# Kernel optimization log

Measured on AMD Instinct MI355X. Metric: run time of the kernel, lower is better.

Reference implementation:

```python
import jax, jax.numpy as jnp
import numpy as np

B, C, H, W = 8, 64, 64, 64
OUT_H, OUT_W = 32, 32


def setup_inputs() -> dict:
    key = jax.random.key(0)
    ks = jax.random.split(key, 9)
    s = 1.0 / np.sqrt(C).astype(np.float32)
    return {
        "x": jax.random.normal(ks[0], (B, C, H, W), jnp.float32),
        "wq": jax.random.normal(ks[1], (C, C), jnp.float32) * s,
        "bq": jax.random.normal(ks[2], (C,), jnp.float32) * 0.01,
        "wk": jax.random.normal(ks[3], (C, C), jnp.float32) * s,
        "bk": jax.random.normal(ks[4], (C,), jnp.float32) * 0.01,
        "wv": jax.random.normal(ks[5], (C, C), jnp.float32) * s,
        "bv": jax.random.normal(ks[6], (C,), jnp.float32) * 0.01,
        "wm": jax.random.normal(ks[7], (C, C), jnp.float32) * s,
        "bm": jax.random.normal(ks[8], (C,), jnp.float32) * 0.01,
    }


def reference(x, wq, bq, wk, bk, wv, bv, wm, bm):
    # pushforward: self-attention over spatial tokens, 1x1-conv mixing + ReLU,
    # then bilinear resize to out_shape (align_corners=False semantics).
    b, c, h, w = x.shape
    t = x.reshape(b, c, h * w).transpose(0, 2, 1)  # [B, HW, C] tokens
    q = jnp.einsum('bnc,dc->bnd', t, wq) + bq      # 1x1 conv == per-pixel linear
    k = jnp.einsum('bnc,dc->bnd', t, wk) + bk
    v = jnp.einsum('bnc,dc->bnd', t, wv) + bv
    scores = jnp.einsum('bnc,bmc->bnm', q, k) / jnp.sqrt(jnp.float32(c))  # [B, HW, HW]
    attn = jax.nn.softmax(scores, axis=-1)
    o = jnp.einsum('bnm,bmc->bnc', attn, v)        # [B, HW, C]
    mixed = jax.nn.relu(jnp.einsum('bnc,dc->bnd', o, wm) + bm)
    out = mixed.transpose(0, 2, 1).reshape(b, c, h, w)
    # F.interpolate(mode='bilinear', align_corners=False) == half-pixel bilinear, no antialias
    out = jax.image.resize(out, (b, c, OUT_H, OUT_W), method='bilinear', antialias=False)
    return out
```

## Files before the change

### kernel.cpp

```cpp
#include <hip/hip_runtime.h>
#include <stdint.h>

typedef unsigned short u16;
typedef unsigned int   u32;
typedef __attribute__((ext_vector_type(8)))  short short8;
typedef __attribute__((ext_vector_type(4)))  float f32x4;
typedef __attribute__((ext_vector_type(16))) float f32x16;

#define NTOK 4096
#define LOG2E 1.44269504088896340736f
#define QS    (0.125f * LOG2E)

__device__ __forceinline__ u16 f2bf(float f) {
    u32 u = __builtin_bit_cast(u32, f);
    u += 0x7fffu + ((u >> 16) & 1u);
    return (u16)(u >> 16);
}
__device__ __forceinline__ float bf2f(u16 v) {
    return __builtin_bit_cast(float, (u32)v << 16);
}
__device__ __forceinline__ u32 pk_hu(float a, float b) {
    u32 ua = __builtin_bit_cast(u32, a) + 0x8000u;
    u32 ub = __builtin_bit_cast(u32, b) + 0x8000u;
    return __builtin_amdgcn_perm(ub, ua, 0x07060302);
}
__device__ __forceinline__ f32x16 zero16() {
    f32x16 v;
#pragma unroll
    for (int i = 0; i < 16; ++i) v[i] = 0.f;
    return v;
}

#define MFMA16x32 __builtin_amdgcn_mfma_f32_16x16x32_bf16
#define MFMA32x16 __builtin_amdgcn_mfma_f32_32x32x16_bf16

__global__ __launch_bounds__(256) void qkv_mfma4(
    const float* __restrict__ x,
    const float* __restrict__ wq, const float* __restrict__ bq,
    const float* __restrict__ wk, const float* __restrict__ bk,
    const float* __restrict__ wv, const float* __restrict__ bv,
    u16* __restrict__ Q, u16* __restrict__ K, u16* __restrict__ Vp)
{
    __shared__ __align__(16) u16 Wl[3 * 64 * 72];
    __shared__ __align__(16) u16 Xl[64 * 64];
    const int tid  = threadIdx.x;
    const int b    = blockIdx.x & 7;
    const int slab = blockIdx.x >> 3;
    const int n0   = slab << 6;
    const int wave = tid >> 6;
    const int lane = tid & 63;
    const int quad = lane >> 4;
    const int l15  = lane & 15;

#pragma unroll
    for (int j = 0; j < 12; ++j) {
        const float* src = (j < 4) ? wq : (j < 8) ? wk : wv;
        const float sc = (j < 4) ? QS : 1.0f;
        const int idx = (j & 3) * 1024 + tid * 4;
        const float4 v = *(const float4*)(src + idx);
        uint2 pk;
        pk.x = (u32)f2bf(v.x * sc) | ((u32)f2bf(v.y * sc) << 16);
        pk.y = (u32)f2bf(v.z * sc) | ((u32)f2bf(v.w * sc) << 16);
        *(uint2*)&Wl[(j >> 2) * 4608 + (idx >> 6) * 72 + (idx & 63)] = pk;
    }

    float4 xs[4];
#pragma unroll
    for (int g = 0; g < 4; ++g) {
        const int ch = g * 16 + wave * 4 + quad;
        xs[g] = *(const float4*)(x + ((size_t)(b * 64 + ch)) * NTOK + n0 + l15 * 4);
    }
#pragma unroll
    for (int g = 0; g < 4; ++g) {
        const int ch = g * 16 + wave * 4 + quad;
        const float vv[4] = {xs[g].x, xs[g].y, xs[g].z, xs[g].w};
#pragma unroll
        for (int e = 0; e < 4; ++e) {
            const int tok = l15 * 4 + e;
            Xl[tok * 64 + (((ch >> 3) ^ (tok & 7)) & 7) * 8 + (ch & 7)] = f2bf(vv[e]);
        }
    }
    __syncthreads();

    const int row0 = wave * 16 + l15;
    short8 xf[2];
#pragma unroll
    for (int kk = 0; kk < 2; ++kk)
        xf[kk] = *(const short8*)&Xl[row0 * 64 + (((kk * 4 + quad) ^ (row0 & 7)) & 7) * 8];

    const size_t tokbase = (size_t)b * NTOK + n0 + wave * 16;

#pragma unroll
    for (int mat = 0; mat < 2; ++mat) {
        const float* bias = (mat == 0) ? bq : bk;
        const float bsc = (mat == 0) ? QS : 1.0f;
#pragma unroll
        for (int mt = 0; mt < 4; ++mt) {
            const u16* wr = &Wl[mat * 4608 + (mt * 16 + l15) * 72 + quad * 8];
            const short8 wf0 = *(const short8*)(wr);
            const short8 wf1 = *(const short8*)(wr + 32);
            f32x4 acc = {0.f, 0.f, 0.f, 0.f};
            acc = MFMA16x32(wf0, xf[0], acc, 0, 0, 0);
            acc = MFMA16x32(wf1, xf[1], acc, 0, 0, 0);
            const float4 b4 = *(const float4*)(bias + mt * 16 + quad * 4);
            uint2 pk;
            pk.x = (u32)f2bf(acc[0] + b4.x * bsc) | ((u32)f2bf(acc[1] + b4.y * bsc) << 16);
            pk.y = (u32)f2bf(acc[2] + b4.z * bsc) | ((u32)f2bf(acc[3] + b4.w * bsc) << 16);
            u16* dst = (mat == 0) ? Q : K;
            *(uint2*)(dst + (tokbase + l15) * 64 + mt * 16 + quad * 4) = pk;
        }
    }

    __syncthreads();
    u16* Vl = Xl;
    const int tok = wave * 16 + l15;
#pragma unroll
    for (int mt = 0; mt < 4; ++mt) {
        const u16* wr = &Wl[2 * 4608 + (mt * 16 + l15) * 72 + quad * 8];
        const short8 wf0 = *(const short8*)(wr);
        const short8 wf1 = *(const short8*)(wr + 32);
        f32x4 acc = {0.f, 0.f, 0.f, 0.f};
        acc = MFMA16x32(wf0, xf[0], acc, 0, 0, 0);
        acc = MFMA16x32(wf1, xf[1], acc, 0, 0, 0);
        const float4 b4 = *(const float4*)(bv + mt * 16 + quad * 4);
        const float o[4] = {acc[0] + b4.x, acc[1] + b4.y, acc[2] + b4.z, acc[3] + b4.w};
#pragma unroll
        for (int r = 0; r < 4; ++r) {
            const int d = mt * 16 + quad * 4 + r;
            Vl[d * 64 + (((tok >> 3) ^ ((d >> 1) & 7)) & 7) * 8 + (tok & 7)] = f2bf(o[r]);
        }
    }
    __syncthreads();

#pragma unroll
    for (int dd = 0; dd < 4; ++dd) {
        const int d2   = (tid >> 4) + dd * 16;
        const int tok0 = (tid & 15) * 4;
        const int slot = ((tok0 >> 3) ^ ((d2 >> 1) & 7)) & 7;
        const uint2 v2 = *(const uint2*)&Vl[d2 * 64 + slot * 8 + (tok0 & 7)];
        const int gt  = slab * 2 + (tok0 >> 5);
        const int tl  = tok0 & 31;
        const int sl  = (tl & 0x13) | (((tl >> 2) & 1) << 3) | (((tl >> 3) & 1) << 2);
        *(uint2*)(Vp + (((size_t)b * 128 + gt) * 64 + d2) * 32 + sl) = v2;
    }
}

__global__ __launch_bounds__(512, 2) void attn8(
    const u16* __restrict__ Q, const u16* __restrict__ K,
    const u16* __restrict__ Vp,
    const float* __restrict__ wm, const float* __restrict__ bm,
    float* __restrict__ out)
{
    __shared__ __align__(16) char smem[54272];
    const int tid  = threadIdx.x;
    const int wave = tid >> 6;
    const int lane = tid & 63;
    const int c31  = lane & 31;
    const int hw   = lane >> 5;
    const int quad = lane >> 4;
    const int l15  = lane & 15;
    const int h    = wave >> 2;
    const int s    = wave & 3;
    const int b    = blockIdx.x & 7;
    const int oh   = blockIdx.x >> 3;
    const int n0   = oh * 128;

    short8 qf[2][4];
#pragma unroll
    for (int nt = 0; nt < 2; ++nt)
#pragma unroll
        for (int ks = 0; ks < 4; ++ks)
            qf[nt][ks] = *(const short8*)(Q + ((size_t)(b * NTOK + n0 + h * 64 + nt * 32 + c31)) * 64
                                            + ks * 16 + hw * 8);

    const u16* Kb  = K + ((size_t)b * NTOK + s * 1024) * 64;
    const u16* Vbp = Vp + ((size_t)b * 128 + s * 32) * 2048;

    f32x16 O[2][2];
#pragma unroll
    for (int mt = 0; mt < 2; ++mt)
#pragma unroll
        for (int nt = 0; nt < 2; ++nt) O[mt][nt] = zero16();
    float lpa[2] = {0.f, 0.f};

    auto load_kv = [&](short8 (&kf)[4], short8 (&vf)[4], int t) {
        const int tc = (t < 32) ? t : 31;
        const u16* kt = Kb + (size_t)tc * 2048;
#pragma unroll
        for (int ks = 0; ks < 4; ++ks)
            kf[ks] = *(const short8*)(kt + c31 * 64 + ks * 16 + hw * 8);
        const u16* vt = Vbp + (size_t)tc * 2048;
#pragma unroll
        for (int mk = 0; mk < 4; ++mk)
            vf[mk] = *(const short8*)(vt + ((mk >> 1) * 32 + c31) * 32 + (mk & 1) * 16 + hw * 8);
    };

    auto S_compute = [&](f32x16 (&sv)[2], const short8 (&kf)[4]) {
#pragma unroll
        for (int nt = 0; nt < 2; ++nt) {
            f32x16 a = zero16();
            a = MFMA32x16(kf[0], qf[nt][0], a, 0, 0, 0);
            a = MFMA32x16(kf[1], qf[nt][1], a, 0, 0, 0);
            a = MFMA32x16(kf[2], qf[nt][2], a, 0, 0, 0);
            a = MFMA32x16(kf[3], qf[nt][3], a, 0, 0, 0);
            sv[nt] = a;
        }
    };

    auto tile_tail = [&](const f32x16 (&sv)[2], const short8 (&vf)[4]) {
#pragma unroll
        for (int nt = 0; nt < 2; ++nt) {
            float p[16];
#pragma unroll
            for (int r = 0; r < 16; ++r) p[r] = __builtin_amdgcn_exp2f(sv[nt][r]);
            lpa[nt] += (((p[0] + p[1]) + (p[2] + p[3])) + ((p[4] + p[5]) + (p[6] + p[7])))
                     + (((p[8] + p[9]) + (p[10] + p[11])) + ((p[12] + p[13]) + (p[14] + p[15])));
            uint4 B0, B1;
            B0.x = pk_hu(p[0],  p[1]);  B0.y = pk_hu(p[2],  p[3]);
            B0.z = pk_hu(p[4],  p[5]);  B0.w = pk_hu(p[6],  p[7]);
            B1.x = pk_hu(p[8],  p[9]);  B1.y = pk_hu(p[10], p[11]);
            B1.z = pk_hu(p[12], p[13]); B1.w = pk_hu(p[14], p[15]);
            const short8 pb0 = __builtin_bit_cast(short8, B0);
            const short8 pb1 = __builtin_bit_cast(short8, B1);
            O[0][nt] = MFMA32x16(vf[0], pb0, O[0][nt], 0, 0, 0);
            O[0][nt] = MFMA32x16(vf[1], pb1, O[0][nt], 0, 0, 0);
            O[1][nt] = MFMA32x16(vf[2], pb0, O[1][nt], 0, 0, 0);
            O[1][nt] = MFMA32x16(vf[3], pb1, O[1][nt], 0, 0, 0);
        }
    };

    short8 kfA[4], vfA[4], kfB[4], vfB[4];
    f32x16 svA[2], svB[2];
    load_kv(kfA, vfA, 0);
    load_kv(kfB, vfB, 1);
    S_compute(svA, kfA);

#pragma unroll 1
    for (int tt = 0; tt < 16; ++tt) {
        const int t0 = tt * 2;
        S_compute(svB, kfB);
        tile_tail(svA, vfA);
        load_kv(kfA, vfA, t0 + 2);
        S_compute(svA, kfA);
        tile_tail(svB, vfB);
        load_kv(kfB, vfB, t0 + 3);
    }

#pragma unroll
    for (int nt = 0; nt < 2; ++nt) lpa[nt] += __shfl_xor(lpa[nt], 32);

    float* lpbuf = (float*)(smem + 52224);
    if (hw == 0) {
#pragma unroll
        for (int nt = 0; nt < 2; ++nt)
            lpbuf[(h * 4 + s) * 64 + nt * 32 + c31] = lpa[nt];
    }
    if (s != 0) {
        u16* sec = (u16*)smem + (h * 3 + s - 1) * 4352;
#pragma unroll
        for (int mt = 0; mt < 2; ++mt)
#pragma unroll
            for (int nt = 0; nt < 2; ++nt)
#pragma unroll
                for (int r = 0; r < 16; ++r) {
                    const int ch = mt * 32 + (r & 3) + 8 * (r >> 2) + 4 * hw;
                    sec[(nt * 32 + c31) * 68 + ch] = f2bf(O[mt][nt][r]);
                }
    }
    __syncthreads();

    float rinv[2];
    if (s == 0) {
#pragma unroll
        for (int nt = 0; nt < 2; ++nt) {
            float sum = 0.f;
#pragma unroll
            for (int sx = 0; sx < 4; ++sx)
                sum += lpbuf[(h * 4 + sx) * 64 + nt * 32 + c31];
            rinv[nt] = 1.0f / sum;
        }
#pragma unroll
        for (int sx = 1; sx < 4; ++sx) {
            const u16* sec = (const u16*)smem + (h * 3 + sx - 1) * 4352;
#pragma unroll
            for (int mt = 0; mt < 2; ++mt)
#pragma unroll
                for (int nt = 0; nt < 2; ++nt)
#pragma unroll
                    for (int r = 0; r < 16; ++r) {
                        const int ch = mt * 32 + (r & 3) + 8 * (r >> 2) + 4 * hw;
                        O[mt][nt][r] += bf2f(sec[(nt * 32 + c31) * 68 + ch]);
                    }
        }
    }
    short8 wB[4][2];
    float bb[4];
#pragma unroll
    for (int nt = 0; nt < 4; ++nt) {
        const int d = nt * 16 + l15;
        const float* wr = wm + (size_t)d * 64 + quad * 8;
        const float4 a0 = *(const float4*)(wr);
        const float4 a1 = *(const float4*)(wr + 4);
        const float4 c0 = *(const float4*)(wr + 32);
        const float4 c1 = *(const float4*)(wr + 36);
        ((u32*)&wB[nt][0])[0] = (u32)f2bf(a0.x) | ((u32)f2bf(a0.y) << 16);
        ((u32*)&wB[nt][0])[1] = (u32)f2bf(a0.z) | ((u32)f2bf(a0.w) << 16);
        ((u32*)&wB[nt][0])[2] = (u32)f2bf(a1.x) | ((u32)f2bf(a1.y) << 16);
        ((u32*)&wB[nt][0])[3] = (u32)f2bf(a1.z) | ((u32)f2bf(a1.w) << 16);
        ((u32*)&wB[nt][1])[0] = (u32)f2bf(c0.x) | ((u32)f2bf(c0.y) << 16);
        ((u32*)&wB[nt][1])[1] = (u32)f2bf(c0.z) | ((u32)f2bf(c0.w) << 16);
        ((u32*)&wB[nt][1])[2] = (u32)f2bf(c1.x) | ((u32)f2bf(c1.y) << 16);
        ((u32*)&wB[nt][1])[3] = (u32)f2bf(c1.z) | ((u32)f2bf(c1.w) << 16);
        bb[nt] = bm[d];
    }
    __syncthreads();

    if (s == 0) {
        u16* M0 = (u16*)smem + h * 4096;
#pragma unroll
        for (int mt = 0; mt < 2; ++mt)
#pragma unroll
            for (int nt = 0; nt < 2; ++nt)
#pragma unroll
                for (int r = 0; r < 16; ++r) {
                    const int lr = nt * 32 + c31;
                    const int ch = mt * 32 + (r & 3) + 8 * (r >> 2) + 4 * hw;
                    const float v = O[mt][nt][r] * rinv[nt];
                    M0[lr * 64 + (((ch >> 3) ^ (lr & 7)) & 7) * 8 + (ch & 7)] = f2bf(v);
                }
    }
    __syncthreads();

    const u16* M0r = (const u16*)smem + (wave >> 2) * 4096;
    const int lr = (wave & 3) * 16 + l15;
    const short8 af0 = *(const short8*)&M0r[lr * 64 + ((quad ^ (lr & 7)) & 7) * 8];
    const short8 af1 = *(const short8*)&M0r[lr * 64 + (((4 + quad) ^ (lr & 7)) & 7) * 8];
    float* Mf = (float*)(smem + 16384);
#pragma unroll
    for (int nt = 0; nt < 4; ++nt) {
        f32x4 acc = {0.f, 0.f, 0.f, 0.f};
        acc = MFMA16x32(af0, wB[nt][0], acc, 0, 0, 0);
        acc = MFMA16x32(af1, wB[nt][1], acc, 0, 0, 0);
#pragma unroll
        for (int r = 0; r < 4; ++r) {
            float v = acc[r] + bb[nt];
            v = v > 0.f ? v : 0.f;
            Mf[(wave * 16 + quad * 4 + r) * 68 + nt * 16 + l15] = v;
        }
    }
    __syncthreads();

    const int ow = tid & 31;
    const int cb = (tid >> 5) & 15;
#pragma unroll
    for (int i = 0; i < 4; ++i) {
        const int c = cb + i * 16;
        const float v = 0.25f * (Mf[(2 * ow) * 68 + c] + Mf[(2 * ow + 1) * 68 + c]
                               + Mf[(64 + 2 * ow) * 68 + c] + Mf[(65 + 2 * ow) * 68 + c]);
        out[((size_t)(b * 64 + c) * 32 + oh) * 32 + ow] = v;
    }
}

extern "C" void kernel_launch(void* const* d_in, const int* in_sizes, int n_in,
                              void* d_out, int out_size, void* d_ws, size_t ws_size,
                              hipStream_t stream) {
    (void)in_sizes; (void)n_in; (void)out_size; (void)ws_size;
    const float* x  = (const float*)d_in[0];
    const float* wq = (const float*)d_in[1];
    const float* bq = (const float*)d_in[2];
    const float* wk = (const float*)d_in[3];
    const float* bk = (const float*)d_in[4];
    const float* wv = (const float*)d_in[5];
    const float* bv = (const float*)d_in[6];
    const float* wm = (const float*)d_in[7];
    const float* bm = (const float*)d_in[8];

    u16* Q  = (u16*)d_ws;
    u16* K  = Q + (size_t)8 * NTOK * 64;
    u16* Vp = K + (size_t)8 * NTOK * 64;

    qkv_mfma4<<<512, 256, 0, stream>>>(x, wq, bq, wk, bk, wv, bv, Q, K, Vp);
    attn8<<<256, 512, 0, stream>>>(Q, K, Vp, wm, bm, (float*)d_out);
}
```

Before: 136.2 us.

## Split attention block into 16 waves each owning 32 query rows

```diff
diff --git a/kernel.cpp b/kernel.cpp
--- a/kernel.cpp
+++ b/kernel.cpp
@@ -145,7 +145,7 @@
     }
 }
 
-__global__ __launch_bounds__(512, 2) void attn8(
+__global__ __launch_bounds__(1024, 4) void attn9(
     const u16* __restrict__ Q, const u16* __restrict__ K,
     const u16* __restrict__ Vp,
     const float* __restrict__ wm, const float* __restrict__ bm,
@@ -165,196 +165,171 @@
     const int oh   = blockIdx.x >> 3;
     const int n0   = oh * 128;
 
-    short8 qf[2][4];
-#pragma unroll
-    for (int nt = 0; nt < 2; ++nt)
-#pragma unroll
-        for (int ks = 0; ks < 4; ++ks)
-            qf[nt][ks] = *(const short8*)(Q + ((size_t)(b * NTOK + n0 + h * 64 + nt * 32 + c31)) * 64
-                                            + ks * 16 + hw * 8);
+    short8 qf[4];
+#pragma unroll
+    for (int ks = 0; ks < 4; ++ks)
+        qf[ks] = *(const short8*)(Q + ((size_t)(b * NTOK + n0 + h * 32 + c31)) * 64
+                                    + ks * 16 + hw * 8);
 
     const u16* Kb  = K + ((size_t)b * NTOK + s * 1024) * 64;
     const u16* Vbp = Vp + ((size_t)b * 128 + s * 32) * 2048;
 
-    f32x16 O[2][2];
-#pragma unroll
-    for (int mt = 0; mt < 2; ++mt)
-#pragma unroll
-        for (int nt = 0; nt < 2; ++nt) O[mt][nt] = zero16();
-    float lpa[2] = {0.f, 0.f};
-
-    auto load_kv = [&](short8 (&kf)[4], short8 (&vf)[4], int t) {
-        const int tc = (t < 32) ? t : 31;
-        const u16* kt = Kb + (size_t)tc * 2048;
+    f32x16 O[2];
+    O[0] = zero16();
+    O[1] = zero16();
+    float lp0 = 0.f, lp1 = 0.f;
+
+    short8 kf[4], vf[4];
+#pragma unroll
+    for (int ks = 0; ks < 4; ++ks)
+        kf[ks] = *(const short8*)(Kb + c31 * 64 + ks * 16 + hw * 8);
+#pragma unroll
+    for (int mk = 0; mk < 4; ++mk)
+        vf[mk] = *(const short8*)(Vbp + ((mk >> 1) * 32 + c31) * 32 + (mk & 1) * 16 + hw * 8);
+
+#pragma unroll 1
+    for (int t = 0; t < 32; ++t) {
+        f32x16 a = zero16();
+        a = MFMA32x16(kf[0], qf[0], a, 0, 0, 0);
+        a = MFMA32x16(kf[1], qf[1], a, 0, 0, 0);
+        a = MFMA32x16(kf[2], qf[2], a, 0, 0, 0);
+        a = MFMA32x16(kf[3], qf[3], a, 0, 0, 0);
+        const int tn = (t + 1 < 32) ? t + 1 : 31;
+        const u16* kt = Kb + (size_t)tn * 2048;
 #pragma unroll
         for (int ks = 0; ks < 4; ++ks)
             kf[ks] = *(const short8*)(kt + c31 * 64 + ks * 16 + hw * 8);
-        const u16* vt = Vbp + (size_t)tc * 2048;
+        uint4 B0, B1;
+        {
+            float p0, p1;
+            p0 = __builtin_amdgcn_exp2f(a[0]);  p1 = __builtin_amdgcn_exp2f(a[1]);
+            B0.x = pk_hu(p0, p1); lp0 += p0 + p1;
+            p0 = __builtin_amdgcn_exp2f(a[2]);  p1 = __builtin_amdgcn_exp2f(a[3]);
+            B0.y = pk_hu(p0, p1); lp1 += p0 + p1;
+            p0 = __builtin_amdgcn_exp2f(a[4]);  p1 = __builtin_amdgcn_exp2f(a[5]);
+            B0.z = pk_hu(p0, p1); lp0 += p0 + p1;
+            p0 = __builtin_amdgcn_exp2f(a[6]);  p1 = __builtin_amdgcn_exp2f(a[7]);
+            B0.w = pk_hu(p0, p1); lp1 += p0 + p1;
+            p0 = __builtin_amdgcn_exp2f(a[8]);  p1 = __builtin_amdgcn_exp2f(a[9]);
+            B1.x = pk_hu(p0, p1); lp0 += p0 + p1;
+            p0 = __builtin_amdgcn_exp2f(a[10]); p1 = __builtin_amdgcn_exp2f(a[11]);
+            B1.y = pk_hu(p0, p1); lp1 += p0 + p1;
+            p0 = __builtin_amdgcn_exp2f(a[12]); p1 = __builtin_amdgcn_exp2f(a[13]);
+            B1.z = pk_hu(p0, p1); lp0 += p0 + p1;
+            p0 = __builtin_amdgcn_exp2f(a[14]); p1 = __builtin_amdgcn_exp2f(a[15]);
+            B1.w = pk_hu(p0, p1); lp1 += p0 + p1;
+        }
+        const short8 pb0 = __builtin_bit_cast(short8, B0);
+        const short8 pb1 = __builtin_bit_cast(short8, B1);
+        O[0] = MFMA32x16(vf[0], pb0, O[0], 0, 0, 0);
+        O[0] = MFMA32x16(vf[1], pb1, O[0], 0, 0, 0);
+        O[1] = MFMA32x16(vf[2], pb0, O[1], 0, 0, 0);
+        O[1] = MFMA32x16(vf[3], pb1, O[1], 0, 0, 0);
+        const u16* vt = Vbp + (size_t)tn * 2048;
 #pragma unroll
         for (int mk = 0; mk < 4; ++mk)
             vf[mk] = *(const short8*)(vt + ((mk >> 1) * 32 + c31) * 32 + (mk & 1) * 16 + hw * 8);
-    };
-
-    auto S_compute = [&](f32x16 (&sv)[2], const short8 (&kf)[4]) {
-#pragma unroll
-        for (int nt = 0; nt < 2; ++nt) {
-            f32x16 a = zero16();
-            a = MFMA32x16(kf[0], qf[nt][0], a, 0, 0, 0);
-            a = MFMA32x16(kf[1], qf[nt][1], a, 0, 0, 0);
-            a = MFMA32x16(kf[2], qf[nt][2], a, 0, 0, 0);
-            a = MFMA32x16(kf[3], qf[nt][3], a, 0, 0, 0);
-            sv[nt] = a;
-        }
-    };
-
-    auto tile_tail = [&](const f32x16 (&sv)[2], const short8 (&vf)[4]) {
-#pragma unroll
-        for (int nt = 0; nt < 2; ++nt) {
-            float p[16];
-#pragma unroll
-            for (int r = 0; r < 16; ++r) p[r] = __builtin_amdgcn_exp2f(sv[nt][r]);
-            lpa[nt] += (((p[0] + p[1]) + (p[2] + p[3])) + ((p[4] + p[5]) + (p[6] + p[7])))
-                     + (((p[8] + p[9]) + (p[10] + p[11])) + ((p[12] + p[13]) + (p[14] + p[15])));
-            uint4 B0, B1;
-            B0.x = pk_hu(p[0],  p[1]);  B0.y = pk_hu(p[2],  p[3]);
-            B0.z = pk_hu(p[4],  p[5]);  B0.w = pk_hu(p[6],  p[7]);
-            B1.x = pk_hu(p[8],  p[9]);  B1.y = pk_hu(p[10], p[11]);
-            B1.z = pk_hu(p[12], p[13]); B1.w = pk_hu(p[14], p[15]);
-            const short8 pb0 = __builtin_bit_cast(short8, B0);
-            const short8 pb1 = __builtin_bit_cast(short8, B1);
-            O[0][nt] = MFMA32x16(vf[0], pb0, O[0][nt], 0, 0, 0);
-            O[0][nt] = MFMA32x16(vf[1], pb1, O[0][nt], 0, 0, 0);
-            O[1][nt] = MFMA32x16(vf[2], pb0, O[1][nt], 0, 0, 0);
-            O[1][nt] = MFMA32x16(vf[3], pb1, O[1][nt], 0, 0, 0);
-        }
-    };
-
-    short8 kfA[4], vfA[4], kfB[4], vfB[4];
-    f32x16 svA[2], svB[2];
-    load_kv(kfA, vfA, 0);
-    load_kv(kfB, vfB, 1);
-    S_compute(svA, kfA);
-
-#pragma unroll 1
-    for (int tt = 0; tt < 16; ++tt) {
-        const int t0 = tt * 2;
-        S_compute(svB, kfB);
-        tile_tail(svA, vfA);
-        load_kv(kfA, vfA, t0 + 2);
-        S_compute(svA, kfA);
-        tile_tail(svB, vfB);
-        load_kv(kfB, vfB, t0 + 3);
-    }
-
-#pragma unroll
-    for (int nt = 0; nt < 2; ++nt) lpa[nt] += __shfl_xor(lpa[nt], 32);
+    }
+
+    float lp = lp0 + lp1;
+    lp += __shfl_xor(lp, 32);
 
     float* lpbuf = (float*)(smem + 52224);
-    if (hw == 0) {
-#pragma unroll
-        for (int nt = 0; nt < 2; ++nt)
-            lpbuf[(h * 4 + s) * 64 + nt * 32 + c31] = lpa[nt];
-    }
+    if (hw == 0) lpbuf[(h * 4 + s) * 32 + c31] = lp;
+
     if (s != 0) {
-        u16* sec = (u16*)smem + (h * 3 + s - 1) * 4352;
+        u16* sec = (u16*)smem + (h * 3 + s - 1) * 2176;
 #pragma unroll
         for (int mt = 0; mt < 2; ++mt)
 #pragma unroll
-            for (int nt = 0; nt < 2; ++nt)
+            for (int r = 0; r < 16; ++r) {
+                const int ch = mt * 32 + (r & 3) + 8 * (r >> 2) + 4 * hw;
+                sec[c31 * 68 + ch] = f2bf(O[mt][r]);
+            }
+    }
+    __syncthreads();
+
+    float rinv = 0.f;
+    if (s == 0) {
+        float sum = 0.f;
+#pragma unroll
+        for (int sx = 0; sx < 4; ++sx)
+            sum += lpbuf[(h * 4 + sx) * 32 + c31];
+        rinv = 1.0f / sum;
+#pragma unroll
+        for (int sx = 1; sx < 4; ++sx) {
+            const u16* sec = (const u16*)smem + (h * 3 + sx - 1) * 2176;
+#pragma unroll
+            for (int mt = 0; mt < 2; ++mt)
 #pragma unroll
                 for (int r = 0; r < 16; ++r) {
                     const int ch = mt * 32 + (r & 3) + 8 * (r >> 2) + 4 * hw;
-                    sec[(nt * 32 + c31) * 68 + ch] = f2bf(O[mt][nt][r]);
+                    O[mt][r] += bf2f(sec[c31 * 68 + ch]);
                 }
-    }
-    __syncthreads();
-
-    float rinv[2];
-    if (s == 0) {
-#pragma unroll
-        for (int nt = 0; nt < 2; ++nt) {
-            float sum = 0.f;
-#pragma unroll
-            for (int sx = 0; sx < 4; ++sx)
-                sum += lpbuf[(h * 4 + sx) * 64 + nt * 32 + c31];
-            rinv[nt] = 1.0f / sum;
-        }
-#pragma unroll
-        for (int sx = 1; sx < 4; ++sx) {
-            const u16* sec = (const u16*)smem + (h * 3 + sx - 1) * 4352;
-#pragma unroll
-            for (int mt = 0; mt < 2; ++mt)
-#pragma unroll
-                for (int nt = 0; nt < 2; ++nt)
-#pragma unroll
-                    for (int r = 0; r < 16; ++r) {
-                        const int ch = mt * 32 + (r & 3) + 8 * (r >> 2) + 4 * hw;
-                        O[mt][nt][r] += bf2f(sec[(nt * 32 + c31) * 68 + ch]);
-                    }
-        }
-    }
-    short8 wB[4][2];
-    float bb[4];
-#pragma unroll
-    for (int nt = 0; nt < 4; ++nt) {
-        const int d = nt * 16 + l15;
+        }
+    }
+    const int rt = wave & 7;
+    const int cH = wave >> 3;
+    short8 wB[2][2];
+    float bb[2];
+#pragma unroll
+    for (int nt2 = 0; nt2 < 2; ++nt2) {
+        const int d = cH * 32 + nt2 * 16 + l15;
         const float* wr = wm + (size_t)d * 64 + quad * 8;
         const float4 a0 = *(const float4*)(wr);
         const float4 a1 = *(const float4*)(wr + 4);
         const float4 c0 = *(const float4*)(wr + 32);
         const float4 c1 = *(const float4*)(wr + 36);
-        ((u32*)&wB[nt][0])[0] = (u32)f2bf(a0.x) | ((u32)f2bf(a0.y) << 16);
-        ((u32*)&wB[nt][0])[1] = (u32)f2bf(a0.z) | ((u32)f2bf(a0.w) << 16);
-        ((u32*)&wB[nt][0])[2] = (u32)f2bf(a1.x) | ((u32)f2bf(a1.y) << 16);
-        ((u32*)&wB[nt][0])[3] = (u32)f2bf(a1.z) | ((u32)f2bf(a1.w) << 16);
-        ((u32*)&wB[nt][1])[0] = (u32)f2bf(c0.x) | ((u32)f2bf(c0.y) << 16);
-        ((u32*)&wB[nt][1])[1] = (u32)f2bf(c0.z) | ((u32)f2bf(c0.w) << 16);
-        ((u32*)&wB[nt][1])[2] = (u32)f2bf(c1.x) | ((u32)f2bf(c1.y) << 16);
-        ((u32*)&wB[nt][1])[3] = (u32)f2bf(c1.z) | ((u32)f2bf(c1.w) << 16);
-        bb[nt] = bm[d];
+        ((u32*)&wB[nt2][0])[0] = (u32)f2bf(a0.x) | ((u32)f2bf(a0.y) << 16);
+        ((u32*)&wB[nt2][0])[1] = (u32)f2bf(a0.z) | ((u32)f2bf(a0.w) << 16);
+        ((u32*)&wB[nt2][0])[2] = (u32)f2bf(a1.x) | ((u32)f2bf(a1.y) << 16);
+        ((u32*)&wB[nt2][0])[3] = (u32)f2bf(a1.z) | ((u32)f2bf(a1.w) << 16);
+        ((u32*)&wB[nt2][1])[0] = (u32)f2bf(c0.x) | ((u32)f2bf(c0.y) << 16);
+        ((u32*)&wB[nt2][1])[1] = (u32)f2bf(c0.z) | ((u32)f2bf(c0.w) << 16);
+        ((u32*)&wB[nt2][1])[2] = (u32)f2bf(c1.x) | ((u32)f2bf(c1.y) << 16);
+        ((u32*)&wB[nt2][1])[3] = (u32)f2bf(c1.z) | ((u32)f2bf(c1.w) << 16);
+        bb[nt2] = bm[d];
     }
     __syncthreads();
 
     if (s == 0) {
-        u16* M0 = (u16*)smem + h * 4096;
+        u16* M0 = (u16*)smem + h * 2048;
 #pragma unroll
         for (int mt = 0; mt < 2; ++mt)
 #pragma unroll
-            for (int nt = 0; nt < 2; ++nt)
-#pragma unroll
-                for (int r = 0; r < 16; ++r) {
-                    const int lr = nt * 32 + c31;
-                    const int ch = mt * 32 + (r & 3) + 8 * (r >> 2) + 4 * hw;
-                    const float v = O[mt][nt][r] * rinv[nt];
-                    M0[lr * 64 + (((ch >> 3) ^ (lr & 7)) & 7) * 8 + (ch & 7)] = f2bf(v);
-                }
-    }
-    __syncthreads();
-
-    const u16* M0r = (const u16*)smem + (wave >> 2) * 4096;
-    const int lr = (wave & 3) * 16 + l15;
+            for (int r = 0; r < 16; ++r) {
+                const int ch = mt * 32 + (r & 3) + 8 * (r >> 2) + 4 * hw;
+                const float v = O[mt][r] * rinv;
+                M0[c31 * 64 + (((ch >> 3) ^ (c31 & 7)) & 7) * 8 + (ch & 7)] = f2bf(v);
+            }
+    }
+    __syncthreads();
+
+    const int row = rt * 16 + l15;
+    const u16* M0r = (const u16*)smem + (row >> 5) * 2048;
+    const int lr = row & 31;
     const short8 af0 = *(const short8*)&M0r[lr * 64 + ((quad ^ (lr & 7)) & 7) * 8];
     const short8 af1 = *(const short8*)&M0r[lr * 64 + (((4 + quad) ^ (lr & 7)) & 7) * 8];
     float* Mf = (float*)(smem + 16384);
 #pragma unroll
-    for (int nt = 0; nt < 4; ++nt) {
+    for (int nt2 = 0; nt2 < 2; ++nt2) {
         f32x4 acc = {0.f, 0.f, 0.f, 0.f};
-        acc = MFMA16x32(af0, wB[nt][0], acc, 0, 0, 0);
-        acc = MFMA16x32(af1, wB[nt][1], acc, 0, 0, 0);
+        acc = MFMA16x32(af0, wB[nt2][0], acc, 0, 0, 0);
+        acc = MFMA16x32(af1, wB[nt2][1], acc, 0, 0, 0);
 #pragma unroll
         for (int r = 0; r < 4; ++r) {
-            float v = acc[r] + bb[nt];
+            float v = acc[r] + bb[nt2];
             v = v > 0.f ? v : 0.f;
-            Mf[(wave * 16 + quad * 4 + r) * 68 + nt * 16 + l15] = v;
+            Mf[(rt * 16 + quad * 4 + r) * 68 + cH * 32 + nt2 * 16 + l15] = v;
         }
     }
     __syncthreads();
 
     const int ow = tid & 31;
-    const int cb = (tid >> 5) & 15;
-#pragma unroll
-    for (int i = 0; i < 4; ++i) {
-        const int c = cb + i * 16;
+    const int c0 = tid >> 5;
+#pragma unroll
+    for (int i = 0; i < 2; ++i) {
+        const int c = c0 + i * 32;
         const float v = 0.25f * (Mf[(2 * ow) * 68 + c] + Mf[(2 * ow + 1) * 68 + c]
                                + Mf[(64 + 2 * ow) * 68 + c] + Mf[(65 + 2 * ow) * 68 + c]);
         out[((size_t)(b * 64 + c) * 32 + oh) * 32 + ow] = v;
@@ -380,5 +355,5 @@
     u16* Vp = K + (size_t)8 * NTOK * 64;
 
     qkv_mfma4<<<512, 256, 0, stream>>>(x, wq, bq, wk, bk, wv, bv, Q, K, Vp);
-    attn8<<<256, 512, 0, stream>>>(Q, K, Vp, wm, bm, (float*)d_out);
-}
+    attn9<<<256, 1024, 0, stream>>>(Q, K, Vp, wm, bm, (float*)d_out);
+}
```

New measurement: 176.6 us. +29.6%, slower.
